# Optimization experiments

Measured on AMD Instinct MI355X. Metric: run time of the kernel, lower is better.

Reference implementation:

```python
import jax, jax.numpy as jnp
import numpy as np

C = 64          # channels
K = 7           # 19 - 6*num with num=2 (conv_first, avg_pool, snake kernel size)
GN_GROUPS = C // 4


def conv2d(x, w, b=None, pad=(0, 0), groups=1):
    out = jax.lax.conv_general_dilated(
        x, w, window_strides=(1, 1),
        padding=((pad[0], pad[0]), (pad[1], pad[1])),
        dimension_numbers=('NCHW', 'OIHW', 'NCHW'),
        feature_group_count=groups)
    if b is not None:
        out = out + b[None, :, None, None]
    return out


def avg_pool(x, k, pad):
    # torch AvgPool2d default count_include_pad=True -> always divide by k*k
    s = jax.lax.reduce_window(x, 0.0, jax.lax.add, (1, 1, k, k), (1, 1, 1, 1),
                              ((0, 0), (0, 0), (pad, pad), (pad, pad)))
    return s / float(k * k)


def bn_eval(x, g, b, m, v, eps):
    inv = g / jnp.sqrt(v + eps)
    return x * inv[None, :, None, None] + (b - m * inv)[None, :, None, None]


def group_norm(x, g, b, groups, eps=1e-5):
    B, Ch, H, W = x.shape
    xr = x.reshape(B, groups, Ch // groups, H, W)
    mu = xr.mean(axis=(2, 3, 4), keepdims=True)
    var = xr.var(axis=(2, 3, 4), keepdims=True)
    xr = (xr - mu) / jnp.sqrt(var + eps)
    return xr.reshape(B, Ch, H, W) * g[None, :, None, None] + b[None, :, None, None]


def cum_offset(off):
    # Faithful to DSCNet DSC: center point pinned to 0, offsets accumulate outward
    # via `for index in range(1, center)`. The two endpoints keep their RAW,
    # DETACHED offsets (original code's off-by-one quirk on the detached clone).
    k = off.shape[1]
    c = k // 2
    new = [None] * k
    new[c] = jnp.zeros_like(off[:, c])
    for i in range(1, c):
        new[c + i] = new[c + i - 1] + off[:, c + i]
        new[c - i] = new[c - i + 1] + off[:, c - i]
    new[0] = jax.lax.stop_gradient(off[:, 0])
    new[k - 1] = jax.lax.stop_gradient(off[:, k - 1])
    return jnp.stack(new, axis=1)


def bilinear(feat, y, x):
    # feat [B,C,R,Cc]; y,x [B,K,R,Cc] -> samples [B,C,K,R,Cc]
    B, Ch, R, Cc = feat.shape
    y0 = jnp.floor(y)
    x0 = jnp.floor(x)
    y0i = jnp.clip(y0.astype(jnp.int32), 0, R - 1)
    y1i = jnp.clip(y0.astype(jnp.int32) + 1, 0, R - 1)
    x0i = jnp.clip(x0.astype(jnp.int32), 0, Cc - 1)
    x1i = jnp.clip(x0.astype(jnp.int32) + 1, 0, Cc - 1)
    gather = jax.vmap(lambda f, yi, xi: f[:, yi, xi])  # [C,R,Cc],[K,R,Cc]->[C,K,R,Cc]
    va0 = gather(feat, y0i, x0i)
    vc0 = gather(feat, y0i, x1i)
    va1 = gather(feat, y1i, x0i)
    vc1 = gather(feat, y1i, x1i)
    # interpolation weights use coords clamped to [0, max+1] (faithful to original)
    y0f = jnp.clip(y0, 0.0, float(R))
    y1f = jnp.clip(y0 + 1.0, 0.0, float(R))
    x0f = jnp.clip(x0, 0.0, float(Cc))
    x1f = jnp.clip(x0 + 1.0, 0.0, float(Cc))
    wa0 = ((y1f - y) * (x1f - x))[:, None]
    wc0 = ((y1f - y) * (x - x0f))[:, None]
    wa1 = ((y - y0f) * (x1f - x))[:, None]
    wc1 = ((y - y0f) * (x - x0f))[:, None]
    return va0 * wa0 + vc0 * wc0 + va1 * wa1 + vc1 * wc1


def dsconv(x, off_w, off_b, bn_g, bn_b, bn_m, bn_v, dsc_w, dsc_b, gn_g, gn_b, morph):
    # Dynamic Snake Conv (extend_scope=1, if_offset=True)
    B, Ch, R, Cc = x.shape
    off = jnp.tanh(bn_eval(conv2d(x, off_w, off_b, (1, 1)), bn_g, bn_b, bn_m, bn_v, 1e-5))
    y_off, x_off = off[:, :K], off[:, K:]
    spread = (jnp.arange(K, dtype=x.dtype) - K // 2)[None, :, None, None]
    rows = jnp.arange(R, dtype=x.dtype)[None, None, :, None]
    cols = jnp.arange(Cc, dtype=x.dtype)[None, None, None, :]
    if morph == 0:  # kernel spreads along x, snake swings in y
        y = rows + cum_offset(y_off)
        xc = cols + spread
    else:           # kernel spreads along y, snake swings in x
        y = rows + spread
        xc = cols + cum_offset(x_off)
    y = jnp.broadcast_to(y, (B, K, R, Cc))
    xc = jnp.broadcast_to(xc, (B, K, R, Cc))
    samp = bilinear(x, y, xc)  # [B,C,K,R,Cc]
    # strided (K,1)/(1,K) conv over the deformed map == contraction over (in, k)
    out = jnp.einsum('oik,bikrc->borc', dsc_w, samp) + dsc_b[None, :, None, None]
    out = group_norm(out, gn_g, gn_b, GN_GROUPS)
    return jax.nn.relu(out)


def setup_inputs() -> dict:
    key = jax.random.key(0)
    kit = iter(jax.random.split(key, 64))

    def rn(shape):
        if len(shape) == 1:
            return jax.random.normal(next(kit), shape, jnp.float32) * 0.05
        fan_in = int(np.prod(shape[1:]))
        return jax.random.normal(next(kit), shape, jnp.float32) / np.sqrt(fan_in)

    B, H, W = 2, 192, 192
    d = {}
    d['x'] = jax.random.normal(next(kit), (B, C, H, W), jnp.float32)
    d['w_first'] = rn((C, C, K, K))
    d['hc1_w'] = rn((C, 1, 1, 9)); d['hc1_b'] = rn((C,))
    d['hc2_w'] = rn((C, 1, 1, 7)); d['hc2_b'] = rn((C,))
    d['hc3_w'] = rn((C, 1, 1, 5)); d['hc3_b'] = rn((C,))
    d['vc1_w'] = rn((C, 1, 9, 1)); d['vc1_b'] = rn((C,))
    d['vc2_w'] = rn((C, 1, 7, 1)); d['vc2_b'] = rn((C,))
    d['vc3_w'] = rn((C, 1, 5, 1)); d['vc3_b'] = rn((C,))
    for p in ('h', 'v'):
        d[p + '_off_w'] = rn((2 * K, C, 3, 3)); d[p + '_off_b'] = rn((2 * K,))
        d[p + '_bn_g'] = 1.0 + rn((2 * K,)); d[p + '_bn_b'] = rn((2 * K,))
        d[p + '_bn_m'] = rn((2 * K,))
        d[p + '_bn_v'] = jax.random.uniform(next(kit), (2 * K,), jnp.float32) + 0.5
        d[p + '_dsc_w'] = rn((C, C, K)); d[p + '_dsc_b'] = rn((C,))
        d[p + '_gn_g'] = 1.0 + rn((C,)); d[p + '_gn_b'] = rn((C,))
    d['last_w'] = rn((C, C, 1, 1))
    d['last_g'] = 1.0 + rn((C,)); d['last_b'] = rn((C,))
    d['last_m'] = rn((C,))
    d['last_v'] = jax.random.uniform(next(kit), (C,), jnp.float32) + 0.5
    return d


def reference(x, w_first, hc1_w, hc1_b, hc2_w, hc2_b, hc3_w, hc3_b,
              vc1_w, vc1_b, vc2_w, vc2_b, vc3_w, vc3_b,
              h_off_w, h_off_b, h_bn_g, h_bn_b, h_bn_m, h_bn_v,
              h_dsc_w, h_dsc_b, h_gn_g, h_gn_b,
              v_off_w, v_off_b, v_bn_g, v_bn_b, v_bn_m, v_bn_v,
              v_dsc_w, v_dsc_b, v_gn_g, v_gn_b,
              last_w, last_g, last_b, last_m, last_v):
    x1 = avg_pool(conv2d(x, w_first, None, (K // 2, K // 2)), K, K // 2)
    h = conv2d(x1, hc1_w, hc1_b, (0, 4), groups=C)
    h = conv2d(h, hc2_w, hc2_b, (0, 3), groups=C)
    h = conv2d(h, hc3_w, hc3_b, (0, 2), groups=C)
    h = dsconv(h, h_off_w, h_off_b, h_bn_g, h_bn_b, h_bn_m, h_bn_v,
               h_dsc_w, h_dsc_b, h_gn_g, h_gn_b, morph=0)
    v = conv2d(x1, vc1_w, vc1_b, (4, 0), groups=C)
    v = conv2d(v, vc2_w, vc2_b, (3, 0), groups=C)
    v = conv2d(v, vc3_w, vc3_b, (2, 0), groups=C)
    v = dsconv(v, v_off_w, v_off_b, v_bn_g, v_bn_b, v_bn_m, v_bn_v,
               v_dsc_w, v_dsc_b, v_gn_g, v_gn_b, morph=1)
    out = h + v + x1
    out = conv2d(out, last_w, None, (0, 0))          # 1x1, bias=False (norm present)
    out = bn_eval(out, last_g, last_b, last_m, last_v, 1e-3)
    return out * jax.nn.sigmoid(out)                  # SiLU
```

## Files before the change

### kernel.cpp

```cpp
#include <hip/hip_runtime.h>
#include <hip/hip_bf16.h>
#include <hip/hip_fp16.h>
#include <math.h>

#define Bq 2
#define Cq 64
#define Hq 192
#define Wq 192
#define HWq (Hq*Wq)
#define Nq ((size_t)Bq*Cq*HWq)

typedef __attribute__((ext_vector_type(8))) _Float16 f16x8;
typedef __attribute__((ext_vector_type(4))) float f32x4;

__device__ inline unsigned short h2us(__half h) {
  union { __half h; unsigned short u; } v; v.h = h; return v.u;
}

__global__ __launch_bounds__(256) void prep_all_kernel(
    const float* hc1_w, const float* hc1_b, const float* hc2_w, const float* hc2_b,
    const float* hc3_w, const float* hc3_b,
    const float* vc1_w, const float* vc1_b, const float* vc2_w, const float* vc2_b,
    const float* vc3_w, const float* vc3_b,
    const float* h_off_w, const float* h_off_b, const float* h_bn_g, const float* h_bn_b,
    const float* h_bn_m, const float* h_bn_v,
    const float* v_off_w, const float* v_off_b, const float* v_bn_g, const float* v_bn_b,
    const float* v_bn_m, const float* v_bn_v,
    const float* last_w, const float* last_g, const float* last_b, const float* last_m,
    const float* last_v,
    const float* __restrict__ w_first,
    const float* __restrict__ h_dsc_w, const float* __restrict__ v_dsc_w,
    float* wEffH, float* bEffH, float* wEffV, float* bEffV,
    float* wOffH, float* bOffH, float* wOffV, float* bOffV,
    float* lwT, float* lbO, float* wB,
    unsigned short* __restrict__ wtpH, unsigned short* __restrict__ wtpV,
    unsigned short* __restrict__ wpack)
{
  int bid = blockIdx.x;
  int t = threadIdx.x;
  if (bid == 0) {
    if (t < 128) {
      int ch = t & 63;
      bool ish = t < 64;
      const float* w1p = (ish ? hc1_w : vc1_w) + ch*9;
      const float* w2p = (ish ? hc2_w : vc2_w) + ch*7;
      const float* w3p = (ish ? hc3_w : vc3_w) + ch*5;
      float w1r[9], w2r[7], w3r[5];
#pragma unroll
      for (int j = 0; j < 9; j++) w1r[j] = w1p[j];
#pragma unroll
      for (int k = 0; k < 7; k++) w2r[k] = w2p[k];
#pragma unroll
      for (int m = 0; m < 5; m++) w3r[m] = w3p[m];
      float t15[15];
#pragma unroll
      for (int s = 0; s < 15; s++) {
        float a = 0.f;
#pragma unroll
        for (int j = 0; j < 9; j++) { int k2 = s - j; if (k2 >= 0 && k2 < 7) a += w1r[j]*w2r[k2]; }
        t15[s] = a;
      }
      float* we = (ish ? wEffH : wEffV) + ch*19;
#pragma unroll
      for (int s = 0; s < 19; s++) {
        float a = 0.f;
#pragma unroll
        for (int j = 0; j < 15; j++) { int k3 = s - j; if (k3 >= 0 && k3 < 5) a += t15[j]*w3r[k3]; }
        we[s] = a;
      }
      float S2 = 0.f, S3 = 0.f;
#pragma unroll
      for (int j = 0; j < 7; j++) S2 += w2r[j];
#pragma unroll
      for (int j = 0; j < 5; j++) S3 += w3r[j];
      float b1 = (ish ? hc1_b : vc1_b)[ch];
      float b2 = (ish ? hc2_b : vc2_b)[ch];
      float b3 = (ish ? hc3_b : vc3_b)[ch];
      (ish ? bEffH : bEffV)[ch] = b1*S2*S3 + b2*S3 + b3;
    }
    for (int idx = t; idx < 9*64*7; idx += 256) {
      int tap = idx / 448; int rem = idx % 448; int i = rem / 7; int m = rem % 7;
      float invh = h_bn_g[m] / sqrtf(h_bn_v[m] + 1e-5f);
      wOffH[(tap*64 + i)*8 + m] = h_off_w[(m*64 + i)*9 + tap] * invh;
      float invv = v_bn_g[7+m] / sqrtf(v_bn_v[7+m] + 1e-5f);
      wOffV[(tap*64 + i)*8 + m] = v_off_w[((7+m)*64 + i)*9 + tap] * invv;
    }
    if (t < 7) {
      float invh = h_bn_g[t] / sqrtf(h_bn_v[t] + 1e-5f);
      bOffH[t] = h_off_b[t]*invh + h_bn_b[t] - h_bn_m[t]*invh;
      float invv = v_bn_g[7+t] / sqrtf(v_bn_v[7+t] + 1e-5f);
      bOffV[t] = v_off_b[7+t]*invv + v_bn_b[7+t] - v_bn_m[7+t]*invv;
    }
    for (int idx = t; idx < 4096; idx += 256) {
      int o = idx % 64; int i = idx / 64;
      float inv = last_g[o] / sqrtf(last_v[o] + 1e-3f);
      lwT[i*64 + o] = last_w[o*64 + i] * inv;
    }
    if (t < 64) {
      float inv = last_g[t] / sqrtf(last_v[t] + 1e-3f);
      lbO[t] = last_b[t] - last_m[t]*inv;
    }
  } else if (bid <= 9) {
    int tid = (bid - 1)*256 + t;
    if (tid >= 2*64*18) return;
    int cls = tid % 18;
    int ch  = (tid / 18) % 64;
    int br  = tid / (18*64);
    int c = (cls < 9) ? cls : cls + 174;
    const float* w1p = (br==0 ? hc1_w : vc1_w) + ch*9;
    const float* w2p = (br==0 ? hc2_w : vc2_w) + ch*7;
    const float* w3p = (br==0 ? hc3_w : vc3_w) + ch*5;
    float b1 = (br==0 ? hc1_b : vc1_b)[ch];
    float b2 = (br==0 ? hc2_b : vc2_b)[ch];
    float b3 = (br==0 ? hc3_b : vc3_b)[ch];
    float w1r[9], w2r[7], w3r[5];
#pragma unroll
    for (int j = 0; j < 9; j++) w1r[j] = w1p[j];
#pragma unroll
    for (int k = 0; k < 7; k++) w2r[k] = w2p[k];
#pragma unroll
    for (int m = 0; m < 5; m++) w3r[m] = w3p[m];
    float acc[19];
#pragma unroll
    for (int s = 0; s < 19; s++) acc[s] = 0.f;
    float bacc = b3;
#pragma unroll
    for (int m = 0; m < 5; m++) {
      int d = c + m - 2;
      bool dok = (d >= 0 && d < Wq);
      float s2b = b2;
#pragma unroll
      for (int k = 0; k < 7; k++) {
        int e = d + k - 3;
        bool eok = (e >= 0 && e < Wq);
        if (eok) s2b += w2r[k] * b1;
        float wmk = w3r[m] * w2r[k];
#pragma unroll
        for (int j = 0; j < 9; j++) {
          int fd = e + j - 4;
          bool fok = (fd >= 0 && fd < Wq);
          float contrib = (dok && eok && fok) ? wmk * w1r[j] : 0.f;
          acc[m + k + j] += contrib;
        }
      }
      if (dok) bacc += w3r[m] * s2b;
    }
    float* dst = wB + ((size_t)(br*64 + ch)*18 + cls)*20;
#pragma unroll
    for (int s = 0; s < 19; s++) dst[s] = acc[s];
    dst[19] = bacc;
  } else {
    int tid = (bid - 10)*256 + t;
    int nthr = 64*256;
    for (int idx = tid; idx < 7*2*2*64*32; idx += nthr) {
      int ch32 = idx & 31;
      int oc   = (idx >> 5) & 63;
      int hl   = (idx >> 11) & 1;
      int kc   = (idx >> 12) & 1;
      int tap  = idx >> 13;
      int i = kc*32 + ch32;
      float vh = h_dsc_w[oc*448 + i*7 + tap];
      float vv = v_dsc_w[oc*448 + i*7 + tap];
      _Float16 hh = (_Float16)vh;
      _Float16 hv = (_Float16)vv;
      unsigned short uh, uv;
      if (!hl) { uh = *(unsigned short*)&hh; uv = *(unsigned short*)&hv; }
      else {
        _Float16 lh = (_Float16)(vh - (float)hh);
        _Float16 lv = (_Float16)(vv - (float)hv);
        uh = *(unsigned short*)&lh; uv = *(unsigned short*)&lv;
      }
      wtpH[idx] = uh; wtpV[idx] = uv;
    }
    for (int e = tid; e < 2*49*2*64*32; e += nthr) {
      int ch  = e & 31;
      int oc  = (e >> 5) & 63;
      int hl  = (e >> 11) & 1;
      int rest = e >> 12;
      int tap = rest % 49;
      int h   = rest / 49;
      float wv = w_first[((size_t)oc*64 + h*32 + ch)*49 + tap];
      __half hh = __float2half(wv);
      unsigned short us;
      if (!hl) us = h2us(hh);
      else { float rr = wv - __half2float(hh); us = h2us(__float2half(rr)); }
      wpack[e] = us;
    }
  }
}

__global__ __launch_bounds__(192) void tof16_pack_kernel(const float* __restrict__ x,
                                                         unsigned short* __restrict__ xpack)
{
  __shared__ unsigned int s[192*64];
  int r = blockIdx.x, b = blockIdx.y;
  int t = threadIdx.x;
  for (int ch = 0; ch < 64; ch++) {
    float v = x[((size_t)(b*64+ch)*Hq + r)*Wq + t];
    _Float16 hh = (_Float16)v;
    s[t*64 + (ch ^ (t & 31))] = (unsigned int)*(unsigned short*)&hh;
  }
  __syncthreads();
  unsigned short* dst = xpack + ((size_t)b*Hq + r)*Wq*64;
  for (int i = 0; i < 8; i++) {
    int gidx = i*192 + t;
    int c = gidx >> 3, g = gidx & 7;
    unsigned short tmp[8];
#pragma unroll
    for (int j = 0; j < 8; j++) {
      int ch = g*8 + j;
      tmp[j] = (unsigned short)s[c*64 + (ch ^ (c & 31))];
    }
    uint4 v;
    v.x = (unsigned int)tmp[0] | ((unsigned int)tmp[1] << 16);
    v.y = (unsigned int)tmp[2] | ((unsigned int)tmp[3] << 16);
    v.z = (unsigned int)tmp[4] | ((unsigned int)tmp[5] << 16);
    v.w = (unsigned int)tmp[6] | ((unsigned int)tmp[7] << 16);
    *(uint4*)(dst + (size_t)gidx*8) = v;
  }
}

__global__ __launch_bounds__(256) void conv7_mfma_kernel(
    const unsigned short* __restrict__ xpack,
    const unsigned short* __restrict__ wpack,
    float* __restrict__ out)
{
  __shared__ __align__(16) unsigned short sA[9*54*32];
  int ct = blockIdx.x;
  int rt = blockIdx.y;
  int b  = blockIdx.z;
  int r0 = rt*3, c0 = ct*48;
  int t = threadIdx.x;
  int wv = t >> 6;
  int l  = t & 63;
  int l15 = l & 15, lg = l >> 4;
  int oc = wv*16 + l15;

  f32x4 acc[3][3];
#pragma unroll
  for (int i = 0; i < 3; i++)
#pragma unroll
    for (int j = 0; j < 3; j++) acc[i][j] = (f32x4){0.f,0.f,0.f,0.f};

  for (int h = 0; h < 2; h++) {
    __syncthreads();
    for (int idx = t; idx < 9*54*4; idx += 256) {
      int g = idx & 3, pix = idx >> 2;
      int row = pix / 54, col = pix % 54;
      int gr = r0 - 3 + row, gc = c0 - 3 + col;
      uint4 v = {0u,0u,0u,0u};
      if (gr >= 0 && gr < Hq && gc >= 0 && gc < Wq)
        v = *(const uint4*)(xpack + (((size_t)b*Hq + gr)*Wq + gc)*64 + (h*4 + g)*8);
      ((uint4*)sA)[(row*54 + col)*4 + (g ^ ((col >> 1) & 3))] = v;
    }
    __syncthreads();
    const unsigned short* wb = wpack + (size_t)h*49*4096;
#pragma unroll 7
    for (int tap = 0; tap < 49; tap++) {
      int dy = tap / 7, dx = tap % 7;
      f16x8 bh = *(const f16x8*)(wb + (size_t)tap*4096 +        oc*32 + lg*8);
      f16x8 bl = *(const f16x8*)(wb + (size_t)tap*4096 + 2048 + oc*32 + lg*8);
#pragma unroll
      for (int rw = 0; rw < 3; rw++) {
        int arow = rw + dy;
        f16x8 a[3];
#pragma unroll
        for (int tc = 0; tc < 3; tc++) {
          int col = tc*16 + l15 + dx;
          a[tc] = *(const f16x8*)((const uint4*)sA + (arow*54 + col)*4 + (lg ^ ((col >> 1) & 3)));
        }
#pragma unroll
        for (int tc = 0; tc < 3; tc++) {
          acc[rw][tc] = __builtin_amdgcn_mfma_f32_16x16x32_f16(a[tc], bh, acc[rw][tc], 0, 0, 0);
          acc[rw][tc] = __builtin_amdgcn_mfma_f32_16x16x32_f16(a[tc], bl, acc[rw][tc], 0, 0, 0);
        }
      }
    }
  }
#pragma unroll
  for (int rw = 0; rw < 3; rw++) {
    float* dst = out + ((size_t)(b*64 + oc)*Hq + (r0 + rw))*Wq + c0;
#pragma unroll
    for (int tc = 0; tc < 3; tc++) {
      f32x4 v = acc[rw][tc];
      *(float4*)(dst + tc*16 + lg*4) = make_float4(v[0], v[1], v[2], v[3]);
    }
  }
}

__global__ __launch_bounds__(256) void pool_fused_kernel(const float* __restrict__ in,
                                                         float* __restrict__ out)
{
  __shared__ float raw[38][192];
  __shared__ float cs[32][192];
  int rt = blockIdx.x;
  int plane = blockIdx.y;
  int r0 = rt*32;
  int t = threadIdx.x;
  const float* src = in + (size_t)plane*HWq;
  for (int idx = t; idx < 38*192; idx += 256) {
    int lr = idx / 192, c = idx % 192;
    int gr = r0 - 3 + lr;
    raw[lr][c] = (gr >= 0 && gr < Hq) ? src[gr*Wq + c] : 0.f;
  }
  __syncthreads();
  for (int idx = t; idx < 32*192; idx += 256) {
    int lr = idx / 192, c = idx % 192;
    float s = 0.f;
#pragma unroll
    for (int dr = 0; dr < 7; dr++) s += raw[lr + dr][c];
    cs[lr][c] = s;
  }
  __syncthreads();
  float* dst = out + (size_t)plane*HWq + r0*Wq;
  for (int idx = t; idx < 32*192; idx += 256) {
    int lr = idx / 192, c = idx % 192;
    float s = 0.f;
#pragma unroll
    for (int dc = -3; dc <= 3; dc++) {
      int cc = c + dc;
      if (cc >= 0 && cc < Wq) s += cs[lr][cc];
    }
    dst[idx] = s * (1.f/49.f);
  }
}

__global__ __launch_bounds__(256) void dwf_kernel(const float* __restrict__ x1,
                                                  const float* __restrict__ wEffH,
                                                  const float* __restrict__ bEffH,
                                                  const float* __restrict__ wBH,
                                                  const float* __restrict__ wEffV,
                                                  const float* __restrict__ bEffV,
                                                  const float* __restrict__ wBV,
                                                  unsigned short* __restrict__ packH,
                                                  unsigned short* __restrict__ packV)
{
  __shared__ float sW[8][19][20];
  int z = blockIdx.z;
  int br = z >> 1, b = z & 1;
  const float* wEff = br ? wEffV : wEffH;
  const float* bEff = br ? bEffV : bEffH;
  const float* wB   = br ? wBV   : wBH;
  unsigned short* pack = br ? packV : packH;
  int g8 = blockIdx.y;
  int t = threadIdx.x;
  int chb = g8*8;
  for (int i = t; i < 8*380; i += 256) {
    int ch8 = i / 380; int rem = i % 380;
    int row = rem / 20, jj = rem % 20;
    int ch = chb + ch8;
    float v;
    if (row < 18) v = wB[((size_t)ch*18 + row)*20 + jj];
    else v = (jj < 19) ? wEff[ch*19 + jj] : bEff[ch];
    sW[ch8][row][jj] = v;
  }
  __syncthreads();
  int p = blockIdx.x*256 + t;
  int r = p / Wq, c = p % Wq;
  float vals[8];
  if (br == 0) {
    int row = (c < 9) ? c : ((c >= Wq-9) ? (c - 174) : 18);
#pragma unroll
    for (int ch8 = 0; ch8 < 8; ch8++) {
      const float* src = x1 + (size_t)(b*Cq + chb + ch8)*HWq + r*Wq;
      float s = sW[ch8][row][19];
#pragma unroll
      for (int j = 0; j < 19; j++) {
        int idx = min(max(c + j - 9, 0), Wq-1);
        s += src[idx] * sW[ch8][row][j];
      }
      vals[ch8] = s;
    }
  } else {
    int row = (r < 9) ? r : ((r >= Hq-9) ? (r - 174) : 18);
#pragma unroll
    for (int ch8 = 0; ch8 < 8; ch8++) {
      const float* src = x1 + (size_t)(b*Cq + chb + ch8)*HWq + c;
      float s = sW[ch8][row][19];
#pragma unroll
      for (int j = 0; j < 19; j++) {
        int idx = min(max(r + j - 9, 0), Hq-1);
        s += src[idx*Wq] * sW[ch8][row][j];
      }
      vals[ch8] = s;
    }
  }
  unsigned int hi[4], lo[4];
#pragma unroll
  for (int q = 0; q < 4; q++) {
    __half h0 = __float2half(vals[2*q]);
    __half h1 = __float2half(vals[2*q+1]);
    __half l0 = __float2half(vals[2*q]   - __half2float(h0));
    __half l1 = __float2half(vals[2*q+1] - __half2float(h1));
    hi[q] = (unsigned int)h2us(h0) | ((unsigned int)h2us(h1) << 16);
    lo[q] = (unsigned int)h2us(l0) | ((unsigned int)h2us(l1) << 16);
  }
  *(uint4*)(pack + (((size_t)b*16 + g8)*HWq + p)*8)     = make_uint4(hi[0], hi[1], hi[2], hi[3]);
  *(uint4*)(pack + (((size_t)b*16 + 8 + g8)*HWq + p)*8) = make_uint4(lo[0], lo[1], lo[2], lo[3]);
}

__global__ __launch_bounds__(256) void off_cum_kernel(const unsigned short* __restrict__ fpH,
                                                      const unsigned short* __restrict__ fpV,
                                                      const float* __restrict__ wOffH,
                                                      const float* __restrict__ bOffH,
                                                      const float* __restrict__ wOffV,
                                                      const float* __restrict__ bOffV,
                                                      float* __restrict__ hcum,
                                                      float* __restrict__ vcum)
{
  const size_t HW8 = (size_t)HWq*8;
  int bid = blockIdx.x;
  int xcd = bid & 7, lid = bid >> 3;
  int combo = xcd >> 1;
  int br = combo >> 1, b = combo & 1;
  int pxblk = (xcd & 1)*72 + lid;
  const unsigned short* fp = br ? fpV : fpH;
  const float* wOff = br ? wOffV : wOffH;
  const float* bOff = br ? bOffV : bOffH;
  float* cum = br ? vcum : hcum;
  int p = pxblk*256 + threadIdx.x;
  int r = p / Wq, c = p % Wq;
  float tv[7];
#pragma unroll
  for (int m = 0; m < 7; m++) tv[m] = bOff[m];
  const unsigned short* fb = fp + (size_t)b*HWq*128;
  for (int tap = 0; tap < 9; tap++) {
    int dy = tap/3 - 1, dx = tap%3 - 1;
    int rr = r + dy, cc = c + dx;
    if (rr < 0 || rr >= Hq || cc < 0 || cc >= Wq) continue;
    const unsigned short* p0 = fb + ((size_t)rr*Wq + cc)*8;
    const float* wp = wOff + tap*512;
    for (int g = 0; g < 8; g++) {
      f16x8 hv = *(const f16x8*)(p0 + (size_t)g*HW8);
      f16x8 lv = *(const f16x8*)(p0 + (size_t)(8 + g)*HW8);
#pragma unroll
      for (int e = 0; e < 8; e++) {
        float fv = (float)hv[e] + (float)lv[e];
        const float* wr = wp + (g*8 + e)*8;
#pragma unroll
        for (int m = 0; m < 7; m++) tv[m] += fv * wr[m];
      }
    }
  }
#pragma unroll
  for (int m = 0; m < 7; m++) tv[m] = tanhf(tv[m]);
  float c0 = tv[0], c1 = tv[1] + tv[2], c2 = tv[2], c3 = 0.f;
  float c4 = tv[4], c5 = tv[4] + tv[5], c6 = tv[6];
  size_t bb = (size_t)b*7*HWq + p;
  cum[bb + 0*HWq] = c0; cum[bb + 1*HWq] = c1; cum[bb + 2*HWq] = c2;
  cum[bb + 3*HWq] = c3; cum[bb + 4*HWq] = c4; cum[bb + 5*HWq] = c5;
  cum[bb + 6*HWq] = c6;
}

__global__ __launch_bounds__(64, 3) void einsum_mfma_kernel(
    const unsigned short* __restrict__ fpH, const unsigned short* __restrict__ fpV,
    const float* __restrict__ cumH, const float* __restrict__ cumV,
    const unsigned short* __restrict__ wtpHp, const unsigned short* __restrict__ wtpVp,
    const float* __restrict__ dscbH, const float* __restrict__ dscbV,
    float* __restrict__ outH, float* __restrict__ outV,
    float* __restrict__ pstat)
{
  __shared__ __align__(16) unsigned short sA[2*32*64];
  const size_t HW8 = (size_t)HWq*8;
  int morph = blockIdx.y;
  const unsigned short* fp  = morph ? fpV   : fpH;
  const float* cum          = morph ? cumV  : cumH;
  const unsigned short* wtp = morph ? wtpVp : wtpHp;
  const float* dsc_b        = morph ? dscbV : dscbH;
  float* out                = morph ? outV  : outH;
  int bid = blockIdx.x;
  int swz = (bid & 7)*288 + (bid >> 3);
  int b   = swz / 1152;
  int blk = swz % 1152;
  int l = threadIdx.x;
  int l15 = l & 15, lg = l >> 4;
  int l7 = l & 7;
  int px5 = l & 31;
  int chh = l >> 5;
  int p = blk*32 + px5;
  int r = p / Wq, c = p % Wq;

  int fixc   = morph ? r : c;
  int vbase  = morph ? c : r;
  int stride = morph ? 1 : Wq;

  f32x4 acc[2][4];
#pragma unroll
  for (int i = 0; i < 2; i++)
#pragma unroll
    for (int j = 0; j < 4; j++) acc[i][j] = (f32x4){0.f,0.f,0.f,0.f};

  const unsigned short* fb = fp + (size_t)b*HWq*128;

  f16x8 a0r[4], a1r[4];
  float w0, w1;
  bool oob;

#define ISSUE(KK)                                                           \
  {                                                                         \
    int fx = fixc + (KK) - 3;                                               \
    oob = (fx < 0 || fx >= 192);                                            \
    float vf = (float)vbase + cum[((size_t)(b*7 + (KK)))*HWq + p];          \
    float v0 = floorf(vf);                                                  \
    int v0q = (int)v0;                                                      \
    int v0i = min(max(v0q, 0), 191);                                        \
    int v1i = min(max(v0q + 1, 0), 191);                                    \
    float v0f = fminf(fmaxf(v0, 0.f), 192.f);                               \
    float v1f = fminf(fmaxf(v0 + 1.f, 0.f), 192.f);                         \
    w0 = v1f - vf; w1 = vf - v0f;                                           \
    int fixoff = morph ? fx*Wq : fx;                                        \
    const unsigned short* p0 = fb + (size_t)(fixoff + v0i*stride)*8;        \
    const unsigned short* p1 = fb + (size_t)(fixoff + v1i*stride)*8;        \
    if (!oob) {                                                             \
      _Pragma("unroll")                                                     \
      for (int gi = 0; gi < 4; gi++) {                                      \
        int g = chh*4 + gi;                                                 \
        a0r[gi] = *(const f16x8*)(p0 + (size_t)g*HW8);                      \
        a1r[gi] = *(const f16x8*)(p1 + (size_t)g*HW8);                      \
      }                                                                     \
    }                                                                       \
  }

#define WRITE(SLOT)                                                         \
  {                                                                         \
    unsigned short* myrow = sA + (size_t)((SLOT)*32 + px5)*64;              \
    if (oob) {                                                              \
      uint4 z = {0u,0u,0u,0u};                                              \
      _Pragma("unroll")                                                     \
      for (int gi = 0; gi < 4; gi++)                                        \
        *(uint4*)(myrow + (size_t)(((chh*4 + gi) ^ l7))*8) = z;             \
    } else {                                                                \
      _Pragma("unroll")                                                     \
      for (int gi = 0; gi < 4; gi++) {                                      \
        f16x8 sh;                                                           \
        _Pragma("unroll")                                                   \
        for (int e = 0; e < 8; e++) {                                       \
          float v = w0*(float)a0r[gi][e] + w1*(float)a1r[gi][e];            \
          sh[e] = (_Float16)v;                                              \
        }                                                                   \
        *(f16x8*)(myrow + (size_t)(((chh*4 + gi) ^ l7))*8) = sh;            \
      }                                                                     \
    }                                                                       \
  }

#define MFMA_TAP(KK, SLOT)                                                  \
  {                                                                         \
    _Pragma("unroll")                                                       \
    for (int kc = 0; kc < 2; kc++) {                                        \
      const unsigned short* wbase = wtp + (size_t)(((KK)*2 + kc)*2)*2048;   \
      f16x8 bh[4], bl[4];                                                   \
      _Pragma("unroll")                                                     \
      for (int tb = 0; tb < 4; tb++) {                                      \
        bh[tb] = *(const f16x8*)(wbase + (tb*16 + l15)*32 + lg*8);          \
        bl[tb] = *(const f16x8*)(wbase + 2048 + (tb*16 + l15)*32 + lg*8);   \
      }                                                                     \
      f16x8 ah[2];                                                          \
      _Pragma("unroll")                                                     \
      for (int ta = 0; ta < 2; ta++) {                                      \
        const unsigned short* rbase = sA + (size_t)((SLOT)*32 + ta*16 + l15)*64; \
        ah[ta] = *(const f16x8*)(rbase + (size_t)((kc*4 + lg) ^ l7)*8);     \
      }                                                                     \
      _Pragma("unroll")                                                     \
      for (int ta = 0; ta < 2; ta++)                                        \
        _Pragma("unroll")                                                   \
        for (int tb = 0; tb < 4; tb++) {                                    \
          acc[ta][tb] = __builtin_amdgcn_mfma_f32_16x16x32_f16(ah[ta], bh[tb], acc[ta][tb], 0, 0, 0); \
          acc[ta][tb] = __builtin_amdgcn_mfma_f32_16x16x32_f16(ah[ta], bl[tb], acc[ta][tb], 0, 0, 0); \
        }                                                                   \
    }                                                                       \
  }

  ISSUE(0);
  WRITE(0);
#pragma unroll 1
  for (int k = 0; k < 7; k++) {
    int slot = k & 1;
    if (k < 6) ISSUE(k+1);
    MFMA_TAP(k, slot);
    if (k < 6) WRITE((k+1) & 1);
  }
#undef ISSUE
#undef WRITE
#undef MFMA_TAP

  int pbase = blk*32;
#pragma unroll
  for (int tb = 0; tb < 4; tb++) {
    int oc = tb*16 + l15;
    float bias = dsc_b[oc];
    float* dst = out + (size_t)(b*64 + oc)*HWq + pbase;
    float s = 0.f, ss = 0.f;
#pragma unroll
    for (int ta = 0; ta < 2; ta++) {
      f32x4 v = acc[ta][tb];
      float v0 = v[0]+bias, v1 = v[1]+bias, v2 = v[2]+bias, v3 = v[3]+bias;
      *(float4*)(dst + ta*16 + lg*4) = make_float4(v0, v1, v2, v3);
      s  += v0 + v1 + v2 + v3;
      ss += v0*v0 + v1*v1 + v2*v2 + v3*v3;
    }
    s  += __shfl_xor(s, 16);
    s  += __shfl_xor(s, 32);
    ss += __shfl_xor(ss, 16);
    ss += __shfl_xor(ss, 32);
    if (lg == 0) {
      float* pp = pstat + ((size_t)(morph*2304 + swz))*128 + oc*2;
      pp[0] = s; pp[1] = ss;
    }
  }
}

__global__ __launch_bounds__(256) void gnred_kernel(const float* __restrict__ pstat,
                                                    float* __restrict__ stats)
{
  int combo = blockIdx.x;
  int buf = combo >> 7;
  int rem = combo & 127;
  int b = rem >> 6, ch = rem & 63;
  int t = threadIdx.x;
  float s = 0.f, ss = 0.f;
  for (int q = t; q < 1152; q += 256) {
    const float* pp = pstat + ((size_t)(buf*2304 + b*1152 + q))*128 + ch*2;
    s += pp[0]; ss += pp[1];
  }
  __shared__ float red[2][4];
  for (int off = 32; off; off >>= 1) {
    s  += __shfl_down(s, off);
    ss += __shfl_down(ss, off);
  }
  if ((t & 63) == 0) { red[0][t >> 6] = s; red[1][t >> 6] = ss; }
  __syncthreads();
  if (t == 0) {
    s  = red[0][0] + red[0][1] + red[0][2] + red[0][3];
    ss = red[1][0] + red[1][1] + red[1][2] + red[1][3];
    stats[combo*2 + 0] = s;
    stats[combo*2 + 1] = ss;
  }
}

__global__ __launch_bounds__(256) void gnfinal_kernel(const float* __restrict__ stats,
                                                      const float* __restrict__ h_gn_g, const float* __restrict__ h_gn_b,
                                                      const float* __restrict__ v_gn_g, const float* __restrict__ v_gn_b,
                                                      float* __restrict__ gnAB)
{
  int t = threadIdx.x;
  int buf = t >> 7, ch = t & 63;
  int base = t & ~3;
  float sum = 0.f, ss = 0.f;
#pragma unroll
  for (int q = 0; q < 4; q++) { sum += stats[(base+q)*2]; ss += stats[(base+q)*2 + 1]; }
  const float n = 4.f * HWq;
  float mean = sum / n;
  float var = ss / n - mean*mean;
  float gg = (buf ? v_gn_g : h_gn_g)[ch];
  float bb = (buf ? v_gn_b : h_gn_b)[ch];
  float A = gg / sqrtf(var + 1e-5f);
  gnAB[t*2 + 0] = A;
  gnAB[t*2 + 1] = bb - mean*A;
}

__global__ __launch_bounds__(256) void final2_kernel(const float* __restrict__ hbuf,
                                                     const float* __restrict__ vbuf,
                                                     const float* __restrict__ x1,
                                                     const float* __restrict__ gnAB,
                                                     const float* __restrict__ lwT,
                                                     const float* __restrict__ lbO,
                                                     float* __restrict__ out)
{
  int b = blockIdx.y;
  int p = blockIdx.x*256 + threadIdx.x;
  float acc[64];
#pragma unroll
  for (int o = 0; o < 64; o++) acc[o] = 0.f;
  for (int i = 0; i < 64; i++) {
    size_t off = (size_t)(b*64 + i)*HWq + p;
    int plane = b*64 + i;
    int ih = plane*2;
    int iv = (128 + plane)*2;
    float hv = fmaxf(hbuf[off]*gnAB[ih] + gnAB[ih+1], 0.f);
    float vv = fmaxf(vbuf[off]*gnAB[iv] + gnAB[iv+1], 0.f);
    float cv = hv + vv + x1[off];
    const float* wr = lwT + i*64;
#pragma unroll
    for (int o = 0; o < 64; o++) acc[o] += cv * wr[o];
  }
  float* dst = out + (size_t)b*Cq*HWq + p;
#pragma unroll
  for (int o = 0; o < 64; o++) {
    float yv = acc[o] + lbO[o];
    dst[(size_t)o*HWq] = yv / (1.f + expf(-yv));
  }
}

extern "C" void kernel_launch(void* const* d_in, const int* in_sizes, int n_in,
                              void* d_out, int out_size, void* d_ws, size_t ws_size,
                              hipStream_t stream)
{
  const float* x       = (const float*)d_in[0];
  const float* w_first = (const float*)d_in[1];
  float* ws = (float*)d_ws;

  float* bufA = ws;
  float* bufB = ws + Nq;
  float* x1   = ws + 2*Nq;
  float* h_ds = ws + 3*Nq;
  float* v_ds = ws + 4*Nq;
  size_t off = 5*Nq;
  float* hcum  = ws + off; off += (size_t)Bq*7*HWq;
  float* vcum  = ws + off; off += (size_t)Bq*7*HWq;
  float* wEffH = ws + off; off += 64*19;
  float* bEffH = ws + off; off += 64;
  float* wEffV = ws + off; off += 64*19;
  float* bEffV = ws + off; off += 64;
  float* wtH   = ws + off; off += 64*64*7;
  float* wtV   = ws + off; off += 64*64*7;
  float* wOffH = ws + off; off += 9*64*8;
  float* bOffH = ws + off; off += 8;
  float* wOffV = ws + off; off += 9*64*8;
  float* bOffV = ws + off; off += 8;
  float* lwT   = ws + off; off += 64*64;
  float* lbO   = ws + off; off += 64;
  float* stats = ws + off; off += 512;
  float* gnAB  = ws + off; off += 512;
  float* wB    = ws + off; off += 2*64*18*20;
  float* pstat = ws + off; off += (size_t)2*2304*128;
  unsigned short* wpack = (unsigned short*)(ws + off); off += 2*49*2*64*32/2 + 16;
  unsigned short* xpack  = (unsigned short*)h_ds;
  unsigned short* fpackH = (unsigned short*)h_ds;
  unsigned short* fpackV = (unsigned short*)v_ds;
  unsigned short* wtpH = (unsigned short*)wtH;
  unsigned short* wtpV = (unsigned short*)wtV;

  prep_all_kernel<<<dim3(74), dim3(256), 0, stream>>>(
      (const float*)d_in[2],  (const float*)d_in[3],  (const float*)d_in[4],  (const float*)d_in[5],
      (const float*)d_in[6],  (const float*)d_in[7],
      (const float*)d_in[8],  (const float*)d_in[9],  (const float*)d_in[10], (const float*)d_in[11],
      (const float*)d_in[12], (const float*)d_in[13],
      (const float*)d_in[14], (const float*)d_in[15], (const float*)d_in[16], (const float*)d_in[17],
      (const float*)d_in[18], (const float*)d_in[19],
      (const float*)d_in[24], (const float*)d_in[25], (const float*)d_in[26], (const float*)d_in[27],
      (const float*)d_in[28], (const float*)d_in[29],
      (const float*)d_in[34], (const float*)d_in[35], (const float*)d_in[36], (const float*)d_in[37],
      (const float*)d_in[38],
      w_first, (const float*)d_in[20], (const float*)d_in[30],
      wEffH, bEffH, wEffV, bEffV, wOffH, bOffH, wOffV, bOffV, lwT, lbO, wB,
      wtpH, wtpV, wpack);

  tof16_pack_kernel<<<dim3(Hq, Bq), dim3(192), 0, stream>>>(x, xpack);
  conv7_mfma_kernel<<<dim3(4, 64, 2), dim3(256), 0, stream>>>(xpack, wpack, bufA);

  pool_fused_kernel<<<dim3(6, 128), dim3(256), 0, stream>>>(bufA, x1);

  dwf_kernel<<<dim3(144, 8, 4), dim3(256), 0, stream>>>(x1, wEffH, bEffH, wB,
      wEffV, bEffV, wB + 64*18*20, fpackH, fpackV);

  off_cum_kernel<<<dim3(576), dim3(256), 0, stream>>>(fpackH, fpackV,
      wOffH, bOffH, wOffV, bOffV, hcum, vcum);

  einsum_mfma_kernel<<<dim3(2304, 2), dim3(64), 0, stream>>>(fpackH, fpackV,
      hcum, vcum, wtpH, wtpV, (const float*)d_in[21], (const float*)d_in[31], bufA, bufB, pstat);

  gnred_kernel<<<dim3(256), dim3(256), 0, stream>>>(pstat, stats);
  gnfinal_kernel<<<dim3(1), dim3(256), 0, stream>>>(stats,
      (const float*)d_in[22], (const float*)d_in[23],
      (const float*)d_in[32], (const float*)d_in[33], gnAB);

  final2_kernel<<<dim3(144, 2), dim3(256), 0, stream>>>(bufA, bufB, x1, gnAB, lwT, lbO, (float*)d_out);
}
```

Measured before the change: 302.7 us.

## Deepen gather prefetch in einsum kernel and shrink conv7 row tile

The deformable einsum kernel now keeps two sets of gather registers, so the global loads for tap k+2 are issued while tap k is being computed. This is meant to hide gather latency better, at the cost of more VGPRs and possibly lower occupancy. Separately, the 7x7 conv tile drops from 3 to 2 rows per block, with the grid raised from 64 to 96 row tiles. That gives more blocks and less LDS per block, but more halo rows are reloaded per output row.

```diff
diff --git a/kernel.cpp b/kernel.cpp
--- a/kernel.cpp
+++ b/kernel.cpp
@@ -225,26 +225,26 @@
     const unsigned short* __restrict__ wpack,
     float* __restrict__ out)
 {
-  __shared__ __align__(16) unsigned short sA[9*54*32];
+  __shared__ __align__(16) unsigned short sA[8*54*32];
   int ct = blockIdx.x;
   int rt = blockIdx.y;
   int b  = blockIdx.z;
-  int r0 = rt*3, c0 = ct*48;
+  int r0 = rt*2, c0 = ct*48;
   int t = threadIdx.x;
   int wv = t >> 6;
   int l  = t & 63;
   int l15 = l & 15, lg = l >> 4;
   int oc = wv*16 + l15;
 
-  f32x4 acc[3][3];
-#pragma unroll
-  for (int i = 0; i < 3; i++)
+  f32x4 acc[2][3];
+#pragma unroll
+  for (int i = 0; i < 2; i++)
 #pragma unroll
     for (int j = 0; j < 3; j++) acc[i][j] = (f32x4){0.f,0.f,0.f,0.f};
 
   for (int h = 0; h < 2; h++) {
     __syncthreads();
-    for (int idx = t; idx < 9*54*4; idx += 256) {
+    for (int idx = t; idx < 8*54*4; idx += 256) {
       int g = idx & 3, pix = idx >> 2;
       int row = pix / 54, col = pix % 54;
       int gr = r0 - 3 + row, gc = c0 - 3 + col;
@@ -261,7 +261,7 @@
       f16x8 bh = *(const f16x8*)(wb + (size_t)tap*4096 +        oc*32 + lg*8);
       f16x8 bl = *(const f16x8*)(wb + (size_t)tap*4096 + 2048 + oc*32 + lg*8);
 #pragma unroll
-      for (int rw = 0; rw < 3; rw++) {
+      for (int rw = 0; rw < 2; rw++) {
         int arow = rw + dy;
         f16x8 a[3];
 #pragma unroll
@@ -278,7 +278,7 @@
     }
   }
 #pragma unroll
-  for (int rw = 0; rw < 3; rw++) {
+  for (int rw = 0; rw < 2; rw++) {
     float* dst = out + ((size_t)(b*64 + oc)*Hq + (r0 + rw))*Wq + c0;
 #pragma unroll
     for (int tc = 0; tc < 3; tc++) {
@@ -492,14 +492,14 @@
 
   const unsigned short* fb = fp + (size_t)b*HWq*128;
 
-  f16x8 a0r[4], a1r[4];
-  float w0, w1;
-  bool oob;
-
-#define ISSUE(KK)                                                           \
+  f16x8 a0A[4], a1A[4], a0B[4], a1B[4];
+  float w0A, w1A, w0B, w1B;
+  bool oobA, oobB;
+
+#define ISSUE(KK, A0R, A1R, W0, W1, OOB)                                    \
   {                                                                         \
     int fx = fixc + (KK) - 3;                                               \
-    oob = (fx < 0 || fx >= 192);                                            \
+    OOB = (fx < 0 || fx >= 192);                                            \
     float vf = (float)vbase + cum[((size_t)(b*7 + (KK)))*HWq + p];          \
     float v0 = floorf(vf);                                                  \
     int v0q = (int)v0;                                                      \
@@ -507,24 +507,24 @@
     int v1i = min(max(v0q + 1, 0), 191);                                    \
     float v0f = fminf(fmaxf(v0, 0.f), 192.f);                               \
     float v1f = fminf(fmaxf(v0 + 1.f, 0.f), 192.f);                         \
-    w0 = v1f - vf; w1 = vf - v0f;                                           \
+    W0 = v1f - vf; W1 = vf - v0f;                                           \
     int fixoff = morph ? fx*Wq : fx;                                        \
     const unsigned short* p0 = fb + (size_t)(fixoff + v0i*stride)*8;        \
     const unsigned short* p1 = fb + (size_t)(fixoff + v1i*stride)*8;        \
-    if (!oob) {                                                             \
+    if (!(OOB)) {                                                           \
       _Pragma("unroll")                                                     \
       for (int gi = 0; gi < 4; gi++) {                                      \
         int g = chh*4 + gi;                                                 \
-        a0r[gi] = *(const f16x8*)(p0 + (size_t)g*HW8);                      \
-        a1r[gi] = *(const f16x8*)(p1 + (size_t)g*HW8);                      \
+        A0R[gi] = *(const f16x8*)(p0 + (size_t)g*HW8);                      \
+        A1R[gi] = *(const f16x8*)(p1 + (size_t)g*HW8);                      \
       }                                                                     \
     }                                                                       \
   }
 
-#define WRITE(SLOT)                                                         \
+#define WRITE(SLOT, A0R, A1R, W0, W1, OOB)                                  \
   {                                                                         \
     unsigned short* myrow = sA + (size_t)((SLOT)*32 + px5)*64;              \
-    if (oob) {                                                              \
+    if (OOB) {                                                              \
       uint4 z = {0u,0u,0u,0u};                                              \
       _Pragma("unroll")                                                     \
       for (int gi = 0; gi < 4; gi++)                                        \
@@ -535,7 +535,7 @@
         f16x8 sh;                                                           \
         _Pragma("unroll")                                                   \
         for (int e = 0; e < 8; e++) {                                       \
-          float v = w0*(float)a0r[gi][e] + w1*(float)a1r[gi][e];            \
+          float v = (W0)*(float)A0R[gi][e] + (W1)*(float)A1R[gi][e];        \
           sh[e] = (_Float16)v;                                              \
         }                                                                   \
         *(f16x8*)(myrow + (size_t)(((chh*4 + gi) ^ l7))*8) = sh;            \
@@ -570,15 +570,20 @@
     }                                                                       \
   }
 
-  ISSUE(0);
-  WRITE(0);
+  ISSUE(0, a0A, a1A, w0A, w1A, oobA);
+  ISSUE(1, a0B, a1B, w0B, w1B, oobB);
+  WRITE(0, a0A, a1A, w0A, w1A, oobA);
 #pragma unroll 1
-  for (int k = 0; k < 7; k++) {
-    int slot = k & 1;
-    if (k < 6) ISSUE(k+1);
-    MFMA_TAP(k, slot);
-    if (k < 6) WRITE((k+1) & 1);
-  }
+  for (int k2 = 0; k2 < 3; k2++) {
+    int k = k2*2;
+    ISSUE(k+2, a0A, a1A, w0A, w1A, oobA);
+    MFMA_TAP(k, 0);
+    WRITE(1, a0B, a1B, w0B, w1B, oobB);
+    if (k2 < 2) ISSUE(k+3, a0B, a1B, w0B, w1B, oobB);
+    MFMA_TAP(k+1, 1);
+    WRITE(0, a0A, a1A, w0A, w1A, oobA);
+  }
+  MFMA_TAP(6, 0);
 #undef ISSUE
 #undef WRITE
 #undef MFMA_TAP
@@ -746,7 +751,7 @@
       wtpH, wtpV, wpack);
 
   tof16_pack_kernel<<<dim3(Hq, Bq), dim3(192), 0, stream>>>(x, xpack);
-  conv7_mfma_kernel<<<dim3(4, 64, 2), dim3(256), 0, stream>>>(xpack, wpack, bufA);
+  conv7_mfma_kernel<<<dim3(4, 96, 2), dim3(256), 0, stream>>>(xpack, wpack, bufA);
 
   pool_fused_kernel<<<dim3(6, 128), dim3(256), 0, stream>>>(bufA, x1);
 
```

Result: no change. 305.7 us (+1.0%).
